# Kernel optimization log

Measured on AMD Instinct MI355X. Metric: run time of the kernel, lower is better.

The kernel has to match this reference:

```python
import jax, jax.numpy as jnp
import numpy as np


def setup_inputs() -> dict:
    key = jax.random.key(0)
    k1, k2, k3 = jax.random.split(key, 3)
    B, D, L = 8, 256, 8192
    inputs = jax.random.normal(k1, (B, D, L), dtype=jnp.float32)
    filters = jax.random.normal(k2, (B, D, L), dtype=jnp.float32)
    # positions in [-1, L); -1 entries are masked out in the output
    positions = jax.random.randint(k3, (B, L), -1, L, dtype=jnp.int64)
    return {"inputs": inputs, "filters": filters, "positions": positions}


def reference(inputs, filters, positions):
    L = inputs.shape[-1]
    n = 2 * L  # zero-pad to 2L for linear (non-circular) convolution
    # torch norm='forward': rfft scaled by 1/n, irfft unscaled
    Xf = jnp.fft.rfft(inputs, n=n, axis=-1, norm="forward")
    Ff = jnp.fft.rfft(filters, n=n, axis=-1, norm="forward")
    result = jnp.fft.irfft(Xf * Ff, n=n, axis=-1, norm="forward")[..., :L]
    mask = (positions != -1).astype(jnp.float32)[:, None, :]  # (B, 1, L)
    return result * mask
```

## Files before the change

### kernel.cpp

```cpp
#include <hip/hip_runtime.h>


#define N_FFT 8192
#define NT    1024
#define NPT   8
#define PI_F  3.14159265358979323846f
#define RS2   0.70710678118654752440f

__device__ __forceinline__ float2 cmul(float2 a, float2 b) {
    return make_float2(a.x * b.x - a.y * b.y, a.x * b.y + a.y * b.x);
}
__device__ __forceinline__ float2 cadd(float2 a, float2 b) { return make_float2(a.x + b.x, a.y + b.y); }
__device__ __forceinline__ float2 csub(float2 a, float2 b) { return make_float2(a.x - b.x, a.y - b.y); }
__device__ __forceinline__ float2 mneg_i(float2 a) { return make_float2(a.y, -a.x); }
__device__ __forceinline__ float2 mpos_i(float2 a) { return make_float2(-a.y, a.x); }

__device__ __forceinline__ int rev13(int v) { return (int)(__brev((unsigned)v) >> 19); }
__device__ __forceinline__ int swz(int i) { return i ^ (((i >> 4) & 7) << 1); }

template <int B>
__device__ __forceinline__ int pass_base(int t) {
    const int lo   = t & ((1 << B) - 1);
    const int hi   = t >> B;
    const int base = (hi << (B + 3)) | lo;
    if constexpr (B == 4) return base;
    else                  return base ^ (((base >> 4) & 7) << 1);
}
template <int B>
__device__ __forceinline__ int pass_addr(int sb, int k) {
    if constexpr (B >= 7)      return sb + (k << B);
    else if constexpr (B == 4) return (sb ^ (k << 1)) + (k << 4);
    else                       return sb ^ (k << 1);
}

template <int B, bool LAST>
__device__ __forceinline__ void fwd_pass(float2* a, int t) {
    const int h  = 1 << B;
    const int lo = t & (h - 1);
    const int sb = pass_base<B>(t);
    float2 r[8];
#pragma unroll
    for (int k = 0; k < 8; ++k) r[k] = a[pass_addr<B>(sb, k)];

    float sn, cs;
    __sincosf(-PI_F * (float)lo / (float)(4 * h), &sn, &cs);
    const float2 T1  = make_float2(cs, sn);
    const float2 T2  = cmul(T1, T1);
    const float2 T4  = cmul(T2, T2);
    const float2 T1b = cmul(T1, make_float2(RS2, -RS2));

#pragma unroll
    for (int k = 0; k < 4; ++k) {
        float2 u = r[k], v = r[k + 4];
        r[k] = cadd(u, v);
        float2 d  = csub(u, v);
        float2 tw = (k == 0) ? T1 : (k == 1) ? T1b : (k == 2) ? mneg_i(T1) : mneg_i(T1b);
        r[k + 4] = cmul(d, tw);
    }
#pragma unroll
    for (int k0 = 0; k0 < 8; k0 += 4) {
#pragma unroll
        for (int kk = 0; kk < 2; ++kk) {
            const int k = k0 + kk;
            float2 u = r[k], v = r[k + 2];
            r[k] = cadd(u, v);
            r[k + 2] = cmul(csub(u, v), kk ? mneg_i(T2) : T2);
        }
    }
#pragma unroll
    for (int k = 0; k < 8; k += 2) {
        float2 u = r[k], v = r[k + 1];
        r[k] = cadd(u, v);
        r[k + 1] = cmul(csub(u, v), T4);
    }
    if (LAST) {
        const float sgn = (t & 1) ? -1.0f : 1.0f;
#pragma unroll
        for (int k = 0; k < 8; ++k) {
            float ox = __shfl_xor(r[k].x, 1);
            float oy = __shfl_xor(r[k].y, 1);
            r[k].x = ox + sgn * r[k].x;
            r[k].y = oy + sgn * r[k].y;
        }
    }
#pragma unroll
    for (int k = 0; k < 8; ++k) a[pass_addr<B>(sb, k)] = r[k];
}

template <int B, bool FIRST, bool STORE>
__device__ __forceinline__ void inv_pass(float2* a, int t, float2 r[8]) {
    const int h  = 1 << B;
    const int lo = t & (h - 1);
    const int sb = pass_base<B>(t);
#pragma unroll
    for (int k = 0; k < 8; ++k) r[k] = a[pass_addr<B>(sb, k)];

    if (FIRST) {
        const float sgn = (t & 1) ? -1.0f : 1.0f;
#pragma unroll
        for (int k = 0; k < 8; ++k) {
            float ox = __shfl_xor(r[k].x, 1);
            float oy = __shfl_xor(r[k].y, 1);
            r[k].x = ox + sgn * r[k].x;
            r[k].y = oy + sgn * r[k].y;
        }
    }
    float sn, cs;
    __sincosf(PI_F * (float)lo / (float)(4 * h), &sn, &cs);
    const float2 U1  = make_float2(cs, sn);
    const float2 U2  = cmul(U1, U1);
    const float2 U4  = cmul(U2, U2);
    const float2 U1b = cmul(U1, make_float2(RS2, RS2));

#pragma unroll
    for (int k = 0; k < 8; k += 2) {
        float2 u = r[k];
        float2 v = cmul(r[k + 1], U4);
        r[k] = cadd(u, v);
        r[k + 1] = csub(u, v);
    }
#pragma unroll
    for (int k0 = 0; k0 < 8; k0 += 4) {
#pragma unroll
        for (int kk = 0; kk < 2; ++kk) {
            const int k = k0 + kk;
            float2 u = r[k];
            float2 v = cmul(r[k + 2], kk ? mpos_i(U2) : U2);
            r[k] = cadd(u, v);
            r[k + 2] = csub(u, v);
        }
    }
#pragma unroll
    for (int k = 0; k < 4; ++k) {
        float2 tw = (k == 0) ? U1 : (k == 1) ? U1b : (k == 2) ? mpos_i(U1) : mpos_i(U1b);
        float2 u = r[k];
        float2 v = cmul(r[k + 4], tw);
        r[k] = cadd(u, v);
        r[k + 4] = csub(u, v);
    }
    if (STORE) {
#pragma unroll
        for (int k = 0; k < 8; ++k) a[pass_addr<B>(sb, k)] = r[k];
    }
}

__device__ __forceinline__ float2 pw(float2 z1, float2 z2, float scale) {
    float2 X = make_float2(0.5f * (z1.x + z2.x), 0.5f * (z1.y - z2.y));
    float2 D = make_float2(z1.x - z2.x, z1.y + z2.y);
    float2 F = make_float2(0.5f * D.y, -0.5f * D.x);
    float2 Y = cmul(X, F);
    return make_float2(Y.x * scale, Y.y * scale);
}

__device__ __forceinline__ float2 gpack(float2 P, float2 Q, float2 E) {
    float2 S  = make_float2(P.x + Q.x, P.y - Q.y);
    float2 Dd = make_float2(P.x - Q.x, P.y + Q.y);
    float2 iE = make_float2(-E.y, E.x);
    return cadd(S, cmul(iE, Dd));
}

__global__ void __launch_bounds__(NT)
fftconv_kernel(const float* __restrict__ x, const float* __restrict__ f,
               const int* __restrict__ pos, float* __restrict__ out) {
    __shared__ float2 A[N_FFT];
    __shared__ float2 Bb[N_FFT];
    const int t   = threadIdx.x;
    const int cch = blockIdx.x;
    const int bb  = cch >> 8;
    const size_t gbase = (size_t)cch * N_FFT;

    const float scale = 1.0f / (16384.0f * 16384.0f);
    const int st = swz(t);
    float2 r[8];

    const float C8[8] = {1.0f, 0.92387953f, 0.70710678f, 0.38268343f,
                         0.0f, -0.38268343f, -0.70710678f, -0.92387953f};
    const float S8[8] = {0.0f, 0.38268343f, 0.70710678f, 0.92387953f,
                         1.0f, 0.92387953f, 0.70710678f, 0.38268343f};

    {
        float sn, cs;
        __sincosf(-PI_F * (float)t / 8192.0f, &sn, &cs);
        const float2 Bt = make_float2(cs, sn);
#pragma unroll
        for (int q = 0; q < NPT; ++q) {
            const int m = q * NT + t;
            const float2 wq = make_float2(x[gbase + m], f[gbase + m]);
            A[st + q * NT] = wq;
            const float2 tw = cmul(Bt, make_float2(C8[q], -S8[q]));
            Bb[st + q * NT] = cmul(wq, tw);
        }
    }
    __syncthreads();

    fwd_pass<10, false>(A, t); fwd_pass<10, false>(Bb, t); __syncthreads();
    fwd_pass<7,  false>(A, t); fwd_pass<7,  false>(Bb, t); __syncthreads();
    fwd_pass<4,  false>(A, t); fwd_pass<4,  false>(Bb, t); __syncthreads();
    fwd_pass<1,  true >(A, t); fwd_pass<1,  true >(Bb, t); __syncthreads();

    {
        float2 Gv[8];
        int    Ga[8];
        const float DC = 0.99999992646f;
        const float DS = 3.83495188e-4f;
#pragma unroll
        for (int q = 0; q < 2; ++q) {
            const int j = (q << 10) | ((t & 7) << 7) | (t >> 3);
            const int b = rev13(j);
            float sn, cs;
            __sincosf(PI_F * (float)j / 4096.0f, &sn, &cs);
            const float2 E  = make_float2(cs, sn);
            const float2 Eo = cmul(E, make_float2(DC, DS));

            if (j == 0) {
                float2 a0 = A[swz(0)], a1 = A[swz(1)], a2 = A[swz(2)], a3 = A[swz(3)];
                float2 P0 = pw(a0, a0, scale);
                float2 Q0 = pw(a1, a1, scale);
                float2 P2 = pw(a2, a3, scale);
                Gv[0] = gpack(P0, Q0, make_float2(1.0f, 0.0f)); Ga[0] = 0;
                Gv[1] = make_float2(2.0f * P2.x, -2.0f * P2.y); Ga[1] = 1;
            } else {
                const int c = rev13(4096 - j);
                float2 z1 = A[swz(b)];
                float2 z2 = A[swz(c + 1)];
                float2 z3 = A[swz(c)];
                float2 z4 = A[swz(b + 1)];
                float2 P = pw(z1, z2, scale);
                float2 Q = pw(z3, z4, scale);
                Gv[q * 4 + 0] = gpack(P, Q, E);                       Ga[q * 4 + 0] = b >> 1;
                Gv[q * 4 + 1] = gpack(Q, P, make_float2(-E.x, E.y));  Ga[q * 4 + 1] = c >> 1;
            }
            {
                const int na = 8191 - b;
                float2 z1 = Bb[swz(b)];
                float2 z2 = Bb[swz(na)];
                float2 z3 = Bb[swz(na - 1)];
                float2 z4 = Bb[swz(b + 1)];
                float2 P = pw(z1, z2, scale);
                float2 Q = pw(z3, z4, scale);
                Gv[q * 4 + 2] = gpack(P, Q, Eo);                        Ga[q * 4 + 2] = (b >> 1) | 4096;
                Gv[q * 4 + 3] = gpack(Q, P, make_float2(-Eo.x, Eo.y));  Ga[q * 4 + 3] = 8191 - (b >> 1);
            }
        }
        __syncthreads();
#pragma unroll
        for (int u = 0; u < 8; ++u) A[swz(Ga[u])] = Gv[u];
    }
    __syncthreads();

    inv_pass<1,  true,  true >(A, t, r); __syncthreads();
    inv_pass<4,  false, true >(A, t, r); __syncthreads();
    inv_pass<7,  false, true >(A, t, r); __syncthreads();
    inv_pass<10, false, false>(A, t, r);

    {
        float2* out2 = (float2*)out + (size_t)cch * 4096;
        const int2* pos2 = (const int2*)(pos) + (size_t)bb * 4096;
#pragma unroll
        for (int k = 0; k < 4; ++k) {
            const int j = k * NT + t;
            const int2 pp = pos2[j];
            const float2 v = r[k];
            out2[j] = make_float2(pp.x != -1 ? v.x : 0.0f,
                                  pp.y != -1 ? v.y : 0.0f);
        }
    }
}

extern "C" void kernel_launch(void* const* d_in, const int* in_sizes, int n_in,
                              void* d_out, int out_size, void* d_ws, size_t ws_size,
                              hipStream_t stream) {
    const float* x   = (const float*)d_in[0];
    const float* f   = (const float*)d_in[1];
    const int*   pos = (const int*)d_in[2];
    float*       out = (float*)d_out;
    (void)in_sizes; (void)n_in; (void)out_size; (void)d_ws; (void)ws_size;

    fftconv_kernel<<<2048, NT, 0, stream>>>(x, f, pos, out);
}
```

Before: 272.6 us.

## Restructure FFT into three radix-32 stages using DPP lane exchanges and fused register-resident first pass

Replaces the four radix-8 shared-memory passes with three stages. The first radix-8 stage runs directly on registers loaded from global memory, and the later stages fold two extra radix-2 levels into each pass using DPP cross-lane moves instead of shared-memory round trips. This removes one LDS read/write pass and one barrier per FFT direction and changes the swizzle pattern to match the new access strides. The trade-off is more complex index arithmetic, re-reading the global inputs for the second buffer, and extra DPP instructions.

```diff
diff --git a/kernel.cpp b/kernel.cpp
--- a/kernel.cpp
+++ b/kernel.cpp
@@ -3,7 +3,6 @@
 
 #define N_FFT 8192
 #define NT    1024
-#define NPT   8
 #define PI_F  3.14159265358979323846f
 #define RS2   0.70710678118654752440f
 
@@ -16,39 +15,22 @@
 __device__ __forceinline__ float2 mpos_i(float2 a) { return make_float2(-a.y, a.x); }
 
 __device__ __forceinline__ int rev13(int v) { return (int)(__brev((unsigned)v) >> 19); }
-__device__ __forceinline__ int swz(int i) { return i ^ (((i >> 4) & 7) << 1); }
-
-template <int B>
-__device__ __forceinline__ int pass_base(int t) {
-    const int lo   = t & ((1 << B) - 1);
-    const int hi   = t >> B;
-    const int base = (hi << (B + 3)) | lo;
-    if constexpr (B == 4) return base;
-    else                  return base ^ (((base >> 4) & 7) << 1);
-}
-template <int B>
-__device__ __forceinline__ int pass_addr(int sb, int k) {
-    if constexpr (B >= 7)      return sb + (k << B);
-    else if constexpr (B == 4) return (sb ^ (k << 1)) + (k << 4);
-    else                       return sb ^ (k << 1);
-}
-
-template <int B, bool LAST>
-__device__ __forceinline__ void fwd_pass(float2* a, int t) {
-    const int h  = 1 << B;
-    const int lo = t & (h - 1);
-    const int sb = pass_base<B>(t);
-    float2 r[8];
-#pragma unroll
-    for (int k = 0; k < 8; ++k) r[k] = a[pass_addr<B>(sb, k)];
-
-    float sn, cs;
-    __sincosf(-PI_F * (float)lo / (float)(4 * h), &sn, &cs);
-    const float2 T1  = make_float2(cs, sn);
+__device__ __forceinline__ int SWZ(int i) { return i ^ (((i >> 5) & 15) << 1); }
+
+__device__ __forceinline__ float dppx1(float v) {
+    return __int_as_float(__builtin_amdgcn_mov_dpp(__float_as_int(v), 0xB1, 0xF, 0xF, true));
+}
+__device__ __forceinline__ float dppx2(float v) {
+    return __int_as_float(__builtin_amdgcn_mov_dpp(__float_as_int(v), 0x4E, 0xF, 0xF, true));
+}
+__device__ __forceinline__ float2 dppx1v(float2 v) { return make_float2(dppx1(v.x), dppx1(v.y)); }
+__device__ __forceinline__ float2 dppx2v(float2 v) { return make_float2(dppx2(v.x), dppx2(v.y)); }
+
+template <bool SH>
+__device__ __forceinline__ void fwd_core(float2 r[8], float2 T1, int t) {
     const float2 T2  = cmul(T1, T1);
     const float2 T4  = cmul(T2, T2);
     const float2 T1b = cmul(T1, make_float2(RS2, -RS2));
-
 #pragma unroll
     for (int k = 0; k < 4; ++k) {
         float2 u = r[k], v = r[k + 4];
@@ -73,45 +55,49 @@
         r[k] = cadd(u, v);
         r[k + 1] = cmul(csub(u, v), T4);
     }
-    if (LAST) {
-        const float sgn = (t & 1) ? -1.0f : 1.0f;
+    if constexpr (SH) {
+        const float2 T8  = cmul(T4, T4);
+        const float2 T16 = cmul(T8, T8);
+        const float2 W2  = make_float2(-T8.x,  -T8.y);
+        const float2 W1  = make_float2(-T16.x, -T16.y);
+        const bool u2 = (t & 2) != 0, u1 = (t & 1) != 0;
 #pragma unroll
         for (int k = 0; k < 8; ++k) {
-            float ox = __shfl_xor(r[k].x, 1);
-            float oy = __shfl_xor(r[k].y, 1);
-            r[k].x = ox + sgn * r[k].x;
-            r[k].y = oy + sgn * r[k].y;
-        }
-    }
-#pragma unroll
-    for (int k = 0; k < 8; ++k) a[pass_addr<B>(sb, k)] = r[k];
-}
-
-template <int B, bool FIRST, bool STORE>
-__device__ __forceinline__ void inv_pass(float2* a, int t, float2 r[8]) {
-    const int h  = 1 << B;
-    const int lo = t & (h - 1);
-    const int sb = pass_base<B>(t);
-#pragma unroll
-    for (int k = 0; k < 8; ++k) r[k] = a[pass_addr<B>(sb, k)];
-
-    if (FIRST) {
-        const float sgn = (t & 1) ? -1.0f : 1.0f;
+            float2 o = dppx2v(r[k]);
+            float2 s = u2 ? csub(o, r[k]) : cadd(r[k], o);
+            r[k] = u2 ? cmul(s, W2) : s;
+        }
 #pragma unroll
         for (int k = 0; k < 8; ++k) {
-            float ox = __shfl_xor(r[k].x, 1);
-            float oy = __shfl_xor(r[k].y, 1);
-            r[k].x = ox + sgn * r[k].x;
-            r[k].y = oy + sgn * r[k].y;
-        }
-    }
-    float sn, cs;
-    __sincosf(PI_F * (float)lo / (float)(4 * h), &sn, &cs);
-    const float2 U1  = make_float2(cs, sn);
-    const float2 U2  = cmul(U1, U1);
-    const float2 U4  = cmul(U2, U2);
+            float2 o = dppx1v(r[k]);
+            float2 s = u1 ? csub(o, r[k]) : cadd(r[k], o);
+            r[k] = u1 ? cmul(s, W1) : s;
+        }
+    }
+}
+
+template <bool SH>
+__device__ __forceinline__ void inv_core(float2 r[8], float2 U1, int t) {
+    const float2 U2 = cmul(U1, U1);
+    const float2 U4 = cmul(U2, U2);
+    if constexpr (SH) {
+        const float2 U8  = cmul(U4, U4);
+        const float2 U16 = cmul(U8, U8);
+        const bool u1 = (t & 1) != 0, u2 = (t & 2) != 0;
+#pragma unroll
+        for (int k = 0; k < 8; ++k) {
+            float2 o = dppx1v(r[k]);
+            float2 m = cmul(U16, u1 ? r[k] : o);
+            r[k] = cadd(u1 ? o : r[k], m);
+        }
+#pragma unroll
+        for (int k = 0; k < 8; ++k) {
+            float2 o = dppx2v(r[k]);
+            float2 m = cmul(U8, u2 ? r[k] : o);
+            r[k] = cadd(u2 ? o : r[k], m);
+        }
+    }
     const float2 U1b = cmul(U1, make_float2(RS2, RS2));
-
 #pragma unroll
     for (int k = 0; k < 8; k += 2) {
         float2 u = r[k];
@@ -137,10 +123,6 @@
         float2 v = cmul(r[k + 4], tw);
         r[k] = cadd(u, v);
         r[k + 4] = csub(u, v);
-    }
-    if (STORE) {
-#pragma unroll
-        for (int k = 0; k < 8; ++k) a[pass_addr<B>(sb, k)] = r[k];
     }
 }
 
@@ -170,33 +152,71 @@
     const size_t gbase = (size_t)cch * N_FFT;
 
     const float scale = 1.0f / (16384.0f * 16384.0f);
-    const int st = swz(t);
     float2 r[8];
+    float sn, cs;
+
+    const int sbR = t ^ (((t >> 5) & 15) << 1);
+    const int sb2 = ((((t >> 7) << 10) | ((t & 3) << 5) | ((t >> 2) & 31))) ^ ((t & 3) << 1);
+    const int kk2[8] = {0, 136, 272, 408, 512, 648, 784, 920};
+    const int sb3 = ((((t >> 2) << 5) | (t & 3))) ^ (((t >> 2) & 15) << 1);
 
     const float C8[8] = {1.0f, 0.92387953f, 0.70710678f, 0.38268343f,
                          0.0f, -0.38268343f, -0.70710678f, -0.92387953f};
     const float S8[8] = {0.0f, 0.38268343f, 0.70710678f, 0.92387953f,
                          1.0f, 0.92387953f, 0.70710678f, 0.38268343f};
-
-    {
-        float sn, cs;
-        __sincosf(-PI_F * (float)t / 8192.0f, &sn, &cs);
-        const float2 Bt = make_float2(cs, sn);
-#pragma unroll
-        for (int q = 0; q < NPT; ++q) {
-            const int m = q * NT + t;
-            const float2 wq = make_float2(x[gbase + m], f[gbase + m]);
-            A[st + q * NT] = wq;
-            const float2 tw = cmul(Bt, make_float2(C8[q], -S8[q]));
-            Bb[st + q * NT] = cmul(wq, tw);
-        }
-    }
-    __syncthreads();
-
-    fwd_pass<10, false>(A, t); fwd_pass<10, false>(Bb, t); __syncthreads();
-    fwd_pass<7,  false>(A, t); fwd_pass<7,  false>(Bb, t); __syncthreads();
-    fwd_pass<4,  false>(A, t); fwd_pass<4,  false>(Bb, t); __syncthreads();
-    fwd_pass<1,  true >(A, t); fwd_pass<1,  true >(Bb, t); __syncthreads();
+    const float lowf = (float)(((t & 3) << 5) | ((t >> 2) & 31));
+
+    __sincosf(-PI_F * (float)t / 4096.0f, &sn, &cs);
+    const float2 T1R = make_float2(cs, sn);
+#pragma unroll
+    for (int k = 0; k < 8; ++k) {
+        const int m = k * NT + t;
+        r[k] = make_float2(x[gbase + m], f[gbase + m]);
+    }
+    fwd_core<false>(r, T1R, t);
+#pragma unroll
+    for (int k = 0; k < 8; ++k) A[sbR + (k << 10)] = r[k];
+    __sincosf(-PI_F * (float)t / 8192.0f, &sn, &cs);
+    const float2 Bt = make_float2(cs, sn);
+#pragma unroll
+    for (int k = 0; k < 8; ++k) {
+        const int m = k * NT + t;
+        const float2 wq = make_float2(x[gbase + m], f[gbase + m]);
+        const float2 tw = cmul(Bt, make_float2(C8[k], -S8[k]));
+        r[k] = cmul(wq, tw);
+    }
+    fwd_core<false>(r, T1R, t);
+#pragma unroll
+    for (int k = 0; k < 8; ++k) Bb[sbR + (k << 10)] = r[k];
+    __syncthreads();
+
+    __sincosf(-PI_F * lowf / 512.0f, &sn, &cs);
+    const float2 L1 = make_float2(cs, sn);
+#pragma unroll
+    for (int k = 0; k < 8; ++k) r[k] = A[sb2 ^ kk2[k]];
+    fwd_core<true>(r, L1, t);
+#pragma unroll
+    for (int k = 0; k < 8; ++k) A[sb2 ^ kk2[k]] = r[k];
+#pragma unroll
+    for (int k = 0; k < 8; ++k) r[k] = Bb[sb2 ^ kk2[k]];
+    fwd_core<true>(r, L1, t);
+#pragma unroll
+    for (int k = 0; k < 8; ++k) Bb[sb2 ^ kk2[k]] = r[k];
+    __syncthreads();
+
+    __sincosf(-PI_F * (float)(t & 3) / 16.0f, &sn, &cs);
+    const float2 M1 = make_float2(cs, sn);
+#pragma unroll
+    for (int k = 0; k < 8; ++k) r[k] = A[sb3 ^ (k << 2)];
+    fwd_core<true>(r, M1, t);
+#pragma unroll
+    for (int k = 0; k < 8; ++k) A[sb3 ^ (k << 2)] = r[k];
+#pragma unroll
+    for (int k = 0; k < 8; ++k) r[k] = Bb[sb3 ^ (k << 2)];
+    fwd_core<true>(r, M1, t);
+#pragma unroll
+    for (int k = 0; k < 8; ++k) Bb[sb3 ^ (k << 2)] = r[k];
+    __syncthreads();
 
     {
         float2 Gv[8];
@@ -207,13 +227,13 @@
         for (int q = 0; q < 2; ++q) {
             const int j = (q << 10) | ((t & 7) << 7) | (t >> 3);
             const int b = rev13(j);
-            float sn, cs;
-            __sincosf(PI_F * (float)j / 4096.0f, &sn, &cs);
-            const float2 E  = make_float2(cs, sn);
+            float sn2, cs2;
+            __sincosf(PI_F * (float)j / 4096.0f, &sn2, &cs2);
+            const float2 E  = make_float2(cs2, sn2);
             const float2 Eo = cmul(E, make_float2(DC, DS));
 
             if (j == 0) {
-                float2 a0 = A[swz(0)], a1 = A[swz(1)], a2 = A[swz(2)], a3 = A[swz(3)];
+                float2 a0 = A[SWZ(0)], a1 = A[SWZ(1)], a2 = A[SWZ(2)], a3 = A[SWZ(3)];
                 float2 P0 = pw(a0, a0, scale);
                 float2 Q0 = pw(a1, a1, scale);
                 float2 P2 = pw(a2, a3, scale);
@@ -221,10 +241,10 @@
                 Gv[1] = make_float2(2.0f * P2.x, -2.0f * P2.y); Ga[1] = 1;
             } else {
                 const int c = rev13(4096 - j);
-                float2 z1 = A[swz(b)];
-                float2 z2 = A[swz(c + 1)];
-                float2 z3 = A[swz(c)];
-                float2 z4 = A[swz(b + 1)];
+                float2 z1 = A[SWZ(b)];
+                float2 z2 = A[SWZ(c + 1)];
+                float2 z3 = A[SWZ(c)];
+                float2 z4 = A[SWZ(b + 1)];
                 float2 P = pw(z1, z2, scale);
                 float2 Q = pw(z3, z4, scale);
                 Gv[q * 4 + 0] = gpack(P, Q, E);                       Ga[q * 4 + 0] = b >> 1;
@@ -232,10 +252,10 @@
             }
             {
                 const int na = 8191 - b;
-                float2 z1 = Bb[swz(b)];
-                float2 z2 = Bb[swz(na)];
-                float2 z3 = Bb[swz(na - 1)];
-                float2 z4 = Bb[swz(b + 1)];
+                float2 z1 = Bb[SWZ(b)];
+                float2 z2 = Bb[SWZ(na)];
+                float2 z3 = Bb[SWZ(na - 1)];
+                float2 z4 = Bb[SWZ(b + 1)];
                 float2 P = pw(z1, z2, scale);
                 float2 Q = pw(z3, z4, scale);
                 Gv[q * 4 + 2] = gpack(P, Q, Eo);                        Ga[q * 4 + 2] = (b >> 1) | 4096;
@@ -244,14 +264,33 @@
         }
         __syncthreads();
 #pragma unroll
-        for (int u = 0; u < 8; ++u) A[swz(Ga[u])] = Gv[u];
-    }
-    __syncthreads();
-
-    inv_pass<1,  true,  true >(A, t, r); __syncthreads();
-    inv_pass<4,  false, true >(A, t, r); __syncthreads();
-    inv_pass<7,  false, true >(A, t, r); __syncthreads();
-    inv_pass<10, false, false>(A, t, r);
+        for (int u = 0; u < 8; ++u) A[SWZ(Ga[u])] = Gv[u];
+    }
+    __syncthreads();
+
+    __sincosf(PI_F * (float)(t & 3) / 16.0f, &sn, &cs);
+    const float2 Mi = make_float2(cs, sn);
+#pragma unroll
+    for (int k = 0; k < 8; ++k) r[k] = A[sb3 ^ (k << 2)];
+    inv_core<true>(r, Mi, t);
+#pragma unroll
+    for (int k = 0; k < 8; ++k) A[sb3 ^ (k << 2)] = r[k];
+    __syncthreads();
+
+    __sincosf(PI_F * lowf / 512.0f, &sn, &cs);
+    const float2 Li = make_float2(cs, sn);
+#pragma unroll
+    for (int k = 0; k < 8; ++k) r[k] = A[sb2 ^ kk2[k]];
+    inv_core<true>(r, Li, t);
+#pragma unroll
+    for (int k = 0; k < 8; ++k) A[sb2 ^ kk2[k]] = r[k];
+    __syncthreads();
+
+    __sincosf(PI_F * (float)t / 4096.0f, &sn, &cs);
+    const float2 Vi = make_float2(cs, sn);
+#pragma unroll
+    for (int k = 0; k < 8; ++k) r[k] = A[sbR + (k << 10)];
+    inv_core<false>(r, Vi, t);
 
     {
         float2* out2 = (float2*)out + (size_t)cch * 4096;
```

Result: slower. 302.1 us (+10.8%).

## Drop second shared FFT buffer by running odd and even FFTs sequentially

Applied to the files above, without the earlier changes.

The two forward FFTs (plain and twisted) now run one after the other through a single 64KB shared buffer, with the odd-half pointwise results kept in registers until the end. This halves LDS use per block so more blocks can be resident per CU. The first radix-8 pass now runs straight from global loads in registers, which removes one LDS round trip and one barrier per FFT. In exchange, the inputs are read from global memory twice and there are more serialized barrier phases per block.

```diff
diff --git a/kernel.cpp b/kernel.cpp
--- a/kernel.cpp
+++ b/kernel.cpp
@@ -33,6 +33,36 @@
     else                       return sb ^ (k << 1);
 }
 
+__device__ __forceinline__ void fwd_core3(float2 r[8], float2 T1) {
+    const float2 T2  = cmul(T1, T1);
+    const float2 T4  = cmul(T2, T2);
+    const float2 T1b = cmul(T1, make_float2(RS2, -RS2));
+#pragma unroll
+    for (int k = 0; k < 4; ++k) {
+        float2 u = r[k], v = r[k + 4];
+        r[k] = cadd(u, v);
+        float2 d  = csub(u, v);
+        float2 tw = (k == 0) ? T1 : (k == 1) ? T1b : (k == 2) ? mneg_i(T1) : mneg_i(T1b);
+        r[k + 4] = cmul(d, tw);
+    }
+#pragma unroll
+    for (int k0 = 0; k0 < 8; k0 += 4) {
+#pragma unroll
+        for (int kk = 0; kk < 2; ++kk) {
+            const int k = k0 + kk;
+            float2 u = r[k], v = r[k + 2];
+            r[k] = cadd(u, v);
+            r[k + 2] = cmul(csub(u, v), kk ? mneg_i(T2) : T2);
+        }
+    }
+#pragma unroll
+    for (int k = 0; k < 8; k += 2) {
+        float2 u = r[k], v = r[k + 1];
+        r[k] = cadd(u, v);
+        r[k + 1] = cmul(csub(u, v), T4);
+    }
+}
+
 template <int B, bool LAST>
 __device__ __forceinline__ void fwd_pass(float2* a, int t) {
     const int h  = 1 << B;
@@ -44,35 +74,8 @@
 
     float sn, cs;
     __sincosf(-PI_F * (float)lo / (float)(4 * h), &sn, &cs);
-    const float2 T1  = make_float2(cs, sn);
-    const float2 T2  = cmul(T1, T1);
-    const float2 T4  = cmul(T2, T2);
-    const float2 T1b = cmul(T1, make_float2(RS2, -RS2));
-
-#pragma unroll
-    for (int k = 0; k < 4; ++k) {
-        float2 u = r[k], v = r[k + 4];
-        r[k] = cadd(u, v);
-        float2 d  = csub(u, v);
-        float2 tw = (k == 0) ? T1 : (k == 1) ? T1b : (k == 2) ? mneg_i(T1) : mneg_i(T1b);
-        r[k + 4] = cmul(d, tw);
-    }
-#pragma unroll
-    for (int k0 = 0; k0 < 8; k0 += 4) {
-#pragma unroll
-        for (int kk = 0; kk < 2; ++kk) {
-            const int k = k0 + kk;
-            float2 u = r[k], v = r[k + 2];
-            r[k] = cadd(u, v);
-            r[k + 2] = cmul(csub(u, v), kk ? mneg_i(T2) : T2);
-        }
-    }
-#pragma unroll
-    for (int k = 0; k < 8; k += 2) {
-        float2 u = r[k], v = r[k + 1];
-        r[k] = cadd(u, v);
-        r[k + 1] = cmul(csub(u, v), T4);
-    }
+    fwd_core3(r, make_float2(cs, sn));
+
     if (LAST) {
         const float sgn = (t & 1) ? -1.0f : 1.0f;
 #pragma unroll
@@ -163,7 +166,6 @@
 fftconv_kernel(const float* __restrict__ x, const float* __restrict__ f,
                const int* __restrict__ pos, float* __restrict__ out) {
     __shared__ float2 A[N_FFT];
-    __shared__ float2 Bb[N_FFT];
     const int t   = threadIdx.x;
     const int cch = blockIdx.x;
     const int bb  = cch >> 8;
@@ -172,79 +174,107 @@
     const float scale = 1.0f / (16384.0f * 16384.0f);
     const int st = swz(t);
     float2 r[8];
+    float2 Godd[4];
+    float sn, cs;
 
     const float C8[8] = {1.0f, 0.92387953f, 0.70710678f, 0.38268343f,
                          0.0f, -0.38268343f, -0.70710678f, -0.92387953f};
     const float S8[8] = {0.0f, 0.38268343f, 0.70710678f, 0.92387953f,
                          1.0f, 0.92387953f, 0.70710678f, 0.38268343f};
-
-    {
-        float sn, cs;
-        __sincosf(-PI_F * (float)t / 8192.0f, &sn, &cs);
-        const float2 Bt = make_float2(cs, sn);
-#pragma unroll
-        for (int q = 0; q < NPT; ++q) {
-            const int m = q * NT + t;
-            const float2 wq = make_float2(x[gbase + m], f[gbase + m]);
-            A[st + q * NT] = wq;
-            const float2 tw = cmul(Bt, make_float2(C8[q], -S8[q]));
-            Bb[st + q * NT] = cmul(wq, tw);
-        }
-    }
-    __syncthreads();
-
-    fwd_pass<10, false>(A, t); fwd_pass<10, false>(Bb, t); __syncthreads();
-    fwd_pass<7,  false>(A, t); fwd_pass<7,  false>(Bb, t); __syncthreads();
-    fwd_pass<4,  false>(A, t); fwd_pass<4,  false>(Bb, t); __syncthreads();
-    fwd_pass<1,  true >(A, t); fwd_pass<1,  true >(Bb, t); __syncthreads();
-
-    {
-        float2 Gv[8];
-        int    Ga[8];
-        const float DC = 0.99999992646f;
-        const float DS = 3.83495188e-4f;
-#pragma unroll
-        for (int q = 0; q < 2; ++q) {
-            const int j = (q << 10) | ((t & 7) << 7) | (t >> 3);
-            const int b = rev13(j);
-            float sn, cs;
-            __sincosf(PI_F * (float)j / 4096.0f, &sn, &cs);
-            const float2 E  = make_float2(cs, sn);
-            const float2 Eo = cmul(E, make_float2(DC, DS));
-
-            if (j == 0) {
-                float2 a0 = A[swz(0)], a1 = A[swz(1)], a2 = A[swz(2)], a3 = A[swz(3)];
-                float2 P0 = pw(a0, a0, scale);
-                float2 Q0 = pw(a1, a1, scale);
-                float2 P2 = pw(a2, a3, scale);
-                Gv[0] = gpack(P0, Q0, make_float2(1.0f, 0.0f)); Ga[0] = 0;
-                Gv[1] = make_float2(2.0f * P2.x, -2.0f * P2.y); Ga[1] = 1;
-            } else {
-                const int c = rev13(4096 - j);
-                float2 z1 = A[swz(b)];
-                float2 z2 = A[swz(c + 1)];
-                float2 z3 = A[swz(c)];
-                float2 z4 = A[swz(b + 1)];
-                float2 P = pw(z1, z2, scale);
-                float2 Q = pw(z3, z4, scale);
-                Gv[q * 4 + 0] = gpack(P, Q, E);                       Ga[q * 4 + 0] = b >> 1;
-                Gv[q * 4 + 1] = gpack(Q, P, make_float2(-E.x, E.y));  Ga[q * 4 + 1] = c >> 1;
-            }
-            {
-                const int na = 8191 - b;
-                float2 z1 = Bb[swz(b)];
-                float2 z2 = Bb[swz(na)];
-                float2 z3 = Bb[swz(na - 1)];
-                float2 z4 = Bb[swz(b + 1)];
-                float2 P = pw(z1, z2, scale);
-                float2 Q = pw(z3, z4, scale);
-                Gv[q * 4 + 2] = gpack(P, Q, Eo);                        Ga[q * 4 + 2] = (b >> 1) | 4096;
-                Gv[q * 4 + 3] = gpack(Q, P, make_float2(-Eo.x, Eo.y));  Ga[q * 4 + 3] = 8191 - (b >> 1);
-            }
-        }
-        __syncthreads();
-#pragma unroll
-        for (int u = 0; u < 8; ++u) A[swz(Ga[u])] = Gv[u];
+    const float DC = 0.99999992646f;
+    const float DS = 3.83495188e-4f;
+
+    __sincosf(-PI_F * (float)t / 4096.0f, &sn, &cs);
+    const float2 T1R = make_float2(cs, sn);
+
+    __sincosf(-PI_F * (float)t / 8192.0f, &sn, &cs);
+    const float2 Bt = make_float2(cs, sn);
+#pragma unroll
+    for (int k = 0; k < 8; ++k) {
+        const int m = k * NT + t;
+        const float2 wq = make_float2(x[gbase + m], f[gbase + m]);
+        const float2 tw = cmul(Bt, make_float2(C8[k], -S8[k]));
+        r[k] = cmul(wq, tw);
+    }
+    fwd_core3(r, T1R);
+#pragma unroll
+    for (int k = 0; k < 8; ++k) A[st + (k << 10)] = r[k];
+    __syncthreads();
+    fwd_pass<7, false>(A, t); __syncthreads();
+    fwd_pass<4, false>(A, t); __syncthreads();
+    fwd_pass<1, true >(A, t); __syncthreads();
+
+#pragma unroll
+    for (int q = 0; q < 2; ++q) {
+        const int j = (q << 10) | ((t & 7) << 7) | (t >> 3);
+        const int b = rev13(j);
+        float sn2, cs2;
+        __sincosf(PI_F * (float)j / 4096.0f, &sn2, &cs2);
+        const float2 E  = make_float2(cs2, sn2);
+        const float2 Eo = cmul(E, make_float2(DC, DS));
+        const int na = 8191 - b;
+        float2 z1 = A[swz(b)];
+        float2 z2 = A[swz(na)];
+        float2 z3 = A[swz(na - 1)];
+        float2 z4 = A[swz(b + 1)];
+        float2 P = pw(z1, z2, scale);
+        float2 Q = pw(z3, z4, scale);
+        Godd[q * 2 + 0] = gpack(P, Q, Eo);
+        Godd[q * 2 + 1] = gpack(Q, P, make_float2(-Eo.x, Eo.y));
+    }
+    __syncthreads();
+
+#pragma unroll
+    for (int k = 0; k < 8; ++k) {
+        const int m = k * NT + t;
+        r[k] = make_float2(x[gbase + m], f[gbase + m]);
+    }
+    fwd_core3(r, T1R);
+#pragma unroll
+    for (int k = 0; k < 8; ++k) A[st + (k << 10)] = r[k];
+    __syncthreads();
+    fwd_pass<7, false>(A, t); __syncthreads();
+    fwd_pass<4, false>(A, t); __syncthreads();
+    fwd_pass<1, true >(A, t); __syncthreads();
+
+    float2 Gev[4];
+    int    Gea[4];
+#pragma unroll
+    for (int q = 0; q < 2; ++q) {
+        const int j = (q << 10) | ((t & 7) << 7) | (t >> 3);
+        const int b = rev13(j);
+        float sn2, cs2;
+        __sincosf(PI_F * (float)j / 4096.0f, &sn2, &cs2);
+        const float2 E = make_float2(cs2, sn2);
+        if (j == 0) {
+            float2 a0 = A[swz(0)], a1 = A[swz(1)], a2 = A[swz(2)], a3 = A[swz(3)];
+            float2 P0 = pw(a0, a0, scale);
+            float2 Q0 = pw(a1, a1, scale);
+            float2 P2 = pw(a2, a3, scale);
+            Gev[0] = gpack(P0, Q0, make_float2(1.0f, 0.0f)); Gea[0] = 0;
+            Gev[1] = make_float2(2.0f * P2.x, -2.0f * P2.y); Gea[1] = 1;
+        } else {
+            const int c = rev13(4096 - j);
+            float2 z1 = A[swz(b)];
+            float2 z2 = A[swz(c + 1)];
+            float2 z3 = A[swz(c)];
+            float2 z4 = A[swz(b + 1)];
+            float2 P = pw(z1, z2, scale);
+            float2 Q = pw(z3, z4, scale);
+            Gev[q * 2 + 0] = gpack(P, Q, E);                      Gea[q * 2 + 0] = b >> 1;
+            Gev[q * 2 + 1] = gpack(Q, P, make_float2(-E.x, E.y)); Gea[q * 2 + 1] = c >> 1;
+        }
+    }
+    __syncthreads();
+
+#pragma unroll
+    for (int u = 0; u < 4; ++u) A[swz(Gea[u])] = Gev[u];
+#pragma unroll
+    for (int q = 0; q < 2; ++q) {
+        const int j = (q << 10) | ((t & 7) << 7) | (t >> 3);
+        const int b = rev13(j);
+        A[swz((b >> 1) | 4096)]  = Godd[q * 2 + 0];
+        A[swz(8191 - (b >> 1))]  = Godd[q * 2 + 1];
     }
     __syncthreads();
 
```

Result: slower. 421.9 us (+54.8%).
